# Kernel tuning notes

Measured on AMD Instinct MI355X. Metric: run time of the kernel, lower is better.

The kernel has to match this reference:

```python
import jax, jax.numpy as jnp
import numpy as np

B, T, G, H = 4, 2048, 1024, 16
HD = G // H  # head dim = 64


def setup_inputs() -> dict:
    key = jax.random.key(0)
    ks = jax.random.split(key, 5)
    s = 1.0 / np.sqrt(G).astype(np.float32)
    return {
        "x": jax.random.normal(ks[0], (B, T, G), jnp.float32),
        "wq": jax.random.normal(ks[1], (G, G), jnp.float32) * s,
        "bq": jnp.zeros((G,), jnp.float32),
        "wk": jax.random.normal(ks[2], (G, G), jnp.float32) * s,
        "bk": jnp.zeros((G,), jnp.float32),
        "wv": jax.random.normal(ks[3], (G, G), jnp.float32) * s,
        "bv": jnp.zeros((G,), jnp.float32),
        "wp": jax.random.normal(ks[4], (G, G), jnp.float32) * s,
        "bp": jnp.zeros((G,), jnp.float32),
    }


def reference(x, wq, bq, wk, bk, wv, bv, wp, bp):
    b, t, g = x.shape
    # QKV projections -> [B, H, T, HD]
    def split_heads(y):
        return y.reshape(b, t, H, HD).transpose(0, 2, 1, 3)
    q = split_heads(x @ wq + bq)
    k = split_heads(x @ wk + bk)
    v = split_heads(x @ wv + bv)
    scale = 1.0 / np.sqrt(HD).astype(np.float32)
    att = jnp.einsum("bhqd,bhkd->bhqk", q, k) * scale  # [B,H,T,T]
    causal = jnp.tril(jnp.ones((t, t), bool))
    att = jnp.where(causal[None, None], att, -jnp.inf)
    att = jax.nn.softmax(att, axis=-1)
    y = jnp.einsum("bhqk,bhkd->bhqd", att, v)  # [B,H,T,HD]
    y = y.transpose(0, 2, 1, 3).reshape(b, t, g)
    return y @ wp + bp
```

## Files before the change

kernel.cpp:

```cpp
#include <hip/hip_runtime.h>
#include <hip/hip_bf16.h>
#include <stdint.h>

typedef unsigned short u16;
typedef __attribute__((ext_vector_type(4))) float f32x4;
typedef __attribute__((ext_vector_type(8))) __bf16 bf16x8;
typedef __attribute__((ext_vector_type(4))) __bf16 bf16x4;
typedef __attribute__((ext_vector_type(4))) unsigned int u32x4;

#define DEV __device__ __forceinline__

DEV u16 f2bf(float f){
  unsigned u = __builtin_bit_cast(unsigned, f);
  u += 0x7fffu + ((u >> 16) & 1u);
  return (u16)(u >> 16);
}

DEV float fexp2(float x){ float r; asm("v_exp_f32 %0, %1" : "=v"(r) : "v"(x)); return r; }

#define GL2LDS(g, l) __builtin_amdgcn_global_load_lds( \
    (const __attribute__((address_space(1))) unsigned int*)(g), \
    (__attribute__((address_space(3))) unsigned int*)(l), 16, 0, 0)

constexpr int Tt = 2048, Gg = 1024, HD = 64;
constexpr float LOG2E = 1.44269504088896340736f;

__global__ __launch_bounds__(256) void k_cvt_x(const float* __restrict__ x, u16* __restrict__ xb){
  long i = (long)blockIdx.x * 256 + threadIdx.x;
  const float4* p = (const float4*)x + 2 * i;
  float4 a = p[0], c = p[1];
  u32x4 v;
  v[0] = (unsigned)f2bf(a.x) | ((unsigned)f2bf(a.y) << 16);
  v[1] = (unsigned)f2bf(a.z) | ((unsigned)f2bf(a.w) << 16);
  v[2] = (unsigned)f2bf(c.x) | ((unsigned)f2bf(c.y) << 16);
  v[3] = (unsigned)f2bf(c.z) | ((unsigned)f2bf(c.w) << 16);
  *(u32x4*)(xb + 8 * i) = v;
}

__global__ void k_transW(const float* __restrict__ wq, const float* __restrict__ wk,
                         const float* __restrict__ wv, const float* __restrict__ wp,
                         u16* __restrict__ wqkvT, u16* __restrict__ wpT){
  __shared__ float tile[32][33];
  int z = blockIdx.z;
  const float* w = (z == 0) ? wq : (z == 1) ? wk : (z == 2) ? wv : wp;
  u16* o = (z < 3) ? (wqkvT + (size_t)z * Gg * Gg) : wpT;
  int n0 = blockIdx.x * 32, k0 = blockIdx.y * 32;
  for (int r = threadIdx.y; r < 32; r += 8)
    tile[r][threadIdx.x] = w[(size_t)(k0 + r) * Gg + n0 + threadIdx.x];
  __syncthreads();
  for (int r = threadIdx.y; r < 32; r += 8)
    o[(size_t)(n0 + r) * Gg + k0 + threadIdx.x] = f2bf(tile[threadIdx.x][r]);
}

template<int EPI>
__global__ __launch_bounds__(256) void k_gemm(
    const u16* __restrict__ A, const u16* __restrict__ Bt, int M, int N, int K,
    const float* __restrict__ b0, const float* __restrict__ b1, const float* __restrict__ b2,
    u16* __restrict__ q_out, u16* __restrict__ k_out, u16* __restrict__ v_out,
    float* __restrict__ out, const float* __restrict__ bp){
  __shared__ u16 lA[2][128 * 32];
  __shared__ u16 lB[2][128 * 32];
  const int tid = threadIdx.x;
  const int lane = tid & 63, w = tid >> 6;
  const int lr = lane & 15, lg = lane >> 4;
  const int wr = w >> 1, wc = w & 1;
  int bid = blockIdx.x;
  int cpx = gridDim.x >> 3;
  int sbid = (bid & 7) * cpx + (bid >> 3);
  const int nbn = N >> 7;
  const int mb = sbid / nbn, nb = sbid % nbn;
  const int m0 = mb * 128, n0 = nb * 128;

  f32x4 acc[4][4];
#pragma unroll
  for (int i = 0; i < 4; i++)
#pragma unroll
    for (int j = 0; j < 4; j++) acc[i][j] = (f32x4)0.f;

  const int lrow = lane >> 2;
  const int lch  = lane & 3;
  const int gswz = (lrow >> 2) & 3;
  const size_t aRow0 = (size_t)(m0 + w * 32 + lrow) * K + (lch ^ gswz) * 8;
  const size_t bRow0 = (size_t)(n0 + w * 32 + lrow) * K + (lch ^ gswz) * 8;

#pragma unroll
  for (int j = 0; j < 2; j++) {
    GL2LDS(A  + aRow0 + (size_t)j * 16 * K, &lA[0][(w * 32 + j * 16) * 32]);
    GL2LDS(Bt + bRow0 + (size_t)j * 16 * K, &lB[0][(w * 32 + j * 16) * 32]);
  }
  __syncthreads();

  int cur = 0;
  for (int k0 = 0; k0 < K; k0 += 32) {
    if (k0 + 32 < K) {
#pragma unroll
      for (int j = 0; j < 2; j++) {
        GL2LDS(A  + aRow0 + (size_t)j * 16 * K + k0 + 32, &lA[cur ^ 1][(w * 32 + j * 16) * 32]);
        GL2LDS(Bt + bRow0 + (size_t)j * 16 * K + k0 + 32, &lB[cur ^ 1][(w * 32 + j * 16) * 32]);
      }
    }
    bf16x8 af[4], bfr[4];
#pragma unroll
    for (int mi = 0; mi < 4; mi++) {
      int row = wr * 64 + mi * 16 + lr;
      int ch = lg ^ ((row >> 2) & 3);
      af[mi] = *(const bf16x8*)&lA[cur][row * 32 + ch * 8];
    }
#pragma unroll
    for (int nj = 0; nj < 4; nj++) {
      int row = wc * 64 + nj * 16 + lr;
      int ch = lg ^ ((row >> 2) & 3);
      bfr[nj] = *(const bf16x8*)&lB[cur][row * 32 + ch * 8];
    }
#pragma unroll
    for (int mi = 0; mi < 4; mi++)
#pragma unroll
      for (int nj = 0; nj < 4; nj++)
        acc[mi][nj] = __builtin_amdgcn_mfma_f32_16x16x32_bf16(af[mi], bfr[nj], acc[mi][nj], 0, 0, 0);

    __syncthreads();
    cur ^= 1;
  }

  if constexpr (EPI == 0) {
#pragma unroll
    for (int nj = 0; nj < 4; nj++) {
      int col = n0 + wc * 64 + nj * 16 + lr;
      int tsel = col >> 10;
      int nn = col & 1023;
      const float* bptr = (tsel == 0) ? b0 : (tsel == 1) ? b1 : b2;
      float bias = bptr[nn];
      int h = nn >> 6, d = nn & 63;
      if (tsel == 2) {
#pragma unroll
        for (int mi = 0; mi < 4; mi++) {
          int rowb = m0 + wr * 64 + mi * 16 + lg * 4;
          int bb = rowb >> 11, t = rowb & 2047;
          int bh = bb * 16 + h;
          ushort4 pk;
          pk.x = f2bf(acc[mi][nj][0] + bias);
          pk.y = f2bf(acc[mi][nj][1] + bias);
          pk.z = f2bf(acc[mi][nj][2] + bias);
          pk.w = f2bf(acc[mi][nj][3] + bias);
          *(ushort4*)&v_out[((size_t)bh * 64 + d) * 2048 + t] = pk;
        }
      } else {
        u16* dst = (tsel == 0) ? q_out : k_out;
        const float sc = (tsel == 0) ? 0.125f * LOG2E : 1.0f;
#pragma unroll
        for (int mi = 0; mi < 4; mi++) {
          int rowb = m0 + wr * 64 + mi * 16 + lg * 4;
#pragma unroll
          for (int r = 0; r < 4; r++) {
            int row = rowb + r;
            int bb = row >> 11, t = row & 2047;
            float v = (acc[mi][nj][r] + bias) * sc;
            dst[((size_t)(bb * 16 + h) * 2048 + t) * 64 + d] = f2bf(v);
          }
        }
      }
    }
  } else {
#pragma unroll
    for (int nj = 0; nj < 4; nj++) {
      int col = n0 + wc * 64 + nj * 16 + lr;
      float bias = bp[col];
#pragma unroll
      for (int mi = 0; mi < 4; mi++) {
#pragma unroll
        for (int r = 0; r < 4; r++) {
          int row = m0 + wr * 64 + mi * 16 + lg * 4 + r;
          out[(size_t)row * 1024 + col] = acc[mi][nj][r] + bias;
        }
      }
    }
  }
}

__global__ __launch_bounds__(512, 4) void k_attn(const u16* __restrict__ Qb, const u16* __restrict__ Kb,
                                                 const u16* __restrict__ Vtb, u16* __restrict__ Ob){
  __shared__ u16 lK[2][64 * 64];
  __shared__ u16 lV[2][64 * 64];
  __shared__ u16 plds[8][1024];
  const int tid = threadIdx.x, lane = tid & 63, w = tid >> 6;
  const int lr = lane & 15, lg = lane >> 4;
  const int slot = blockIdx.x & 255;
  const int rr = blockIdx.x >> 8;
  const int bh = slot & 63;
  const int g  = slot >> 6;
  const int qb = (rr == 0) ? 7 - g : g;
  const int q0w = qb * 256 + w * 32;
  const int b = bh >> 4, h = bh & 15;
  const size_t base  = (size_t)bh * Tt * HD;
  const size_t vbase = (size_t)bh * HD * Tt;
  char* pw = (char*)&plds[w][0];

  const int sl3 = lane >> 3, sc = lane & 7;
  const int r0 = w * 8;
  const int srow = r0 + sl3;
  const int schk = (sc ^ (srow & 7)) * 8;

  bf16x8 qf[2][2];
#pragma unroll
  for (int qg = 0; qg < 2; qg++)
#pragma unroll
    for (int dh = 0; dh < 2; dh++)
      qf[qg][dh] = *(const bf16x8*)(Qb + base + (size_t)(q0w + qg * 16 + lr) * 64 + dh * 32 + lg * 8);

  f32x4 Oacc[2][4];
#pragma unroll
  for (int qg = 0; qg < 2; qg++)
#pragma unroll
    for (int nf = 0; nf < 4; nf++) Oacc[qg][nf] = (f32x4)0.f;
  float mrun[2] = {-__builtin_inff(), -__builtin_inff()};
  float lsum[2] = {0.f, 0.f};

  const int ntile = 4 * qb + 4;

  GL2LDS(Kb + base + (size_t)srow * 64 + schk, &lK[0][r0 * 64]);
  GL2LDS(Vtb + vbase + (size_t)srow * Tt + schk, &lV[0][r0 * 64]);
  __syncthreads();

  int cur = 0;
  for (int kt = 0; kt < ntile; kt++) {
    const int kv0 = kt << 6;
    if (kt + 1 < ntile) {
      const int nkv0 = kv0 + 64;
      GL2LDS(Kb + base + (size_t)(nkv0 + srow) * 64 + schk, &lK[cur ^ 1][r0 * 64]);
      GL2LDS(Vtb + vbase + (size_t)srow * Tt + nkv0 + schk, &lV[cur ^ 1][r0 * 64]);
    }

    if (kv0 <= q0w + 31) {
      const bool full = (kv0 + 63 <= q0w);
      const u16* lKc = &lK[cur][0];
      const u16* lVc = &lV[cur][0];

      f32x4 accs[4][2];
#pragma unroll
      for (int kg = 0; kg < 4; kg++) {
        int row = kg * 16 + lr;
        bf16x8 kf0 = *(const bf16x8*)&lKc[row * 64 + (lg ^ (row & 7)) * 8];
        bf16x8 kf1 = *(const bf16x8*)&lKc[row * 64 + ((4 + lg) ^ (row & 7)) * 8];
#pragma unroll
        for (int qg = 0; qg < 2; qg++) {
          accs[kg][qg] = __builtin_amdgcn_mfma_f32_16x16x32_bf16(kf0, qf[qg][0], (f32x4)0.f, 0, 0, 0);
          accs[kg][qg] = __builtin_amdgcn_mfma_f32_16x16x32_bf16(kf1, qf[qg][1], accs[kg][qg], 0, 0, 0);
        }
      }

      float pvv[2][4][4];
#pragma unroll
      for (int qg = 0; qg < 2; qg++) {
        const int q = q0w + qg * 16 + lr;
        float tm = -__builtin_inff();
#pragma unroll
        for (int kg = 0; kg < 4; kg++)
#pragma unroll
          for (int r = 0; r < 4; r++) {
            float s = accs[kg][qg][r];
            if (!full) { int kv = kv0 + kg * 16 + lg * 4 + r; if (kv > q) s = -__builtin_inff(); }
            pvv[qg][kg][r] = s;
            tm = fmaxf(tm, s);
          }
        if (!__all(tm <= mrun[qg] + 8.f)) {
          float tmr = fmaxf(tm, __shfl_xor(tm, 16));
          tmr = fmaxf(tmr, __shfl_xor(tmr, 32));
          float mnew = fmaxf(mrun[qg], tmr);
          float alpha = fexp2(mrun[qg] - mnew);
          mrun[qg] = mnew;
          lsum[qg] *= alpha;
#pragma unroll
          for (int r = 0; r < 4; r++) {
            float aO = __shfl(alpha, lg * 4 + r);
#pragma unroll
            for (int nf = 0; nf < 4; nf++) Oacc[qg][nf][r] *= aO;
          }
        }
        const float m = mrun[qg];
        float ps = 0.f;
#pragma unroll
        for (int kg = 0; kg < 4; kg++)
#pragma unroll
          for (int r = 0; r < 4; r++) {
            float p = fexp2(pvv[qg][kg][r] - m);
            pvv[qg][kg][r] = p;
            ps += p;
          }
        lsum[qg] += ps;
      }

      bf16x8 vfr[2][4];
      const int rs = lr & 7;
#pragma unroll
      for (int qg = 0; qg < 2; qg++) {
#pragma unroll
        for (int kg = 0; kg < 4; kg++) {
          int chunk = kg * 2 + (lg >> 1);
          int byte = lr * 128 + ((chunk ^ rs) << 4) + (lg & 1) * 8;
          bf16x4 t;
          t[0] = (__bf16)pvv[qg][kg][0]; t[1] = (__bf16)pvv[qg][kg][1];
          t[2] = (__bf16)pvv[qg][kg][2]; t[3] = (__bf16)pvv[qg][kg][3];
          *(bf16x4*)(pw + byte) = t;
        }
#pragma unroll
        for (int ks = 0; ks < 2; ks++) {
          bf16x8 pf = *(const bf16x8*)(pw + lr * 128 + (((ks * 4 + lg) ^ rs) << 4));
#pragma unroll
          for (int nf = 0; nf < 4; nf++) {
            if (qg == 0) {
              int vrow = nf * 16 + lr;
              vfr[ks][nf] = *(const bf16x8*)&lVc[vrow * 64 + ((ks * 4 + lg) ^ (vrow & 7)) * 8];
            }
            Oacc[qg][nf] = __builtin_amdgcn_mfma_f32_16x16x32_bf16(pf, vfr[ks][nf], Oacc[qg][nf], 0, 0, 0);
          }
        }
      }
    }

    __syncthreads();
    cur ^= 1;
  }

#pragma unroll
  for (int qg = 0; qg < 2; qg++) {
    float ls = lsum[qg];
    ls += __shfl_xor(ls, 16);
    ls += __shfl_xor(ls, 32);
    float li = 1.f / ls;
#pragma unroll
    for (int r = 0; r < 4; r++) {
      float liO = __shfl(li, lg * 4 + r);
      int q = q0w + qg * 16 + lg * 4 + r;
      size_t rowoff = ((size_t)b * Tt + q) * Gg + h * 64;
#pragma unroll
      for (int nf = 0; nf < 4; nf++)
        Ob[rowoff + nf * 16 + lr] = f2bf(Oacc[qg][nf][r] * liO);
    }
  }
}

extern "C" void kernel_launch(void* const* d_in, const int* in_sizes, int n_in,
                              void* d_out, int out_size, void* d_ws, size_t ws_size,
                              hipStream_t stream){
  const float* x  = (const float*)d_in[0];
  const float* wq = (const float*)d_in[1];
  const float* bq = (const float*)d_in[2];
  const float* wk = (const float*)d_in[3];
  const float* bk = (const float*)d_in[4];
  const float* wv = (const float*)d_in[5];
  const float* bv = (const float*)d_in[6];
  const float* wp = (const float*)d_in[7];
  const float* bp = (const float*)d_in[8];
  float* out = (float*)d_out;
  char* ws = (char*)d_ws;

  u16* xb    = (u16*)(ws);
  u16* wqkvT = (u16*)(ws + (16l << 20));
  u16* wpT   = (u16*)(ws + (22l << 20));
  u16* Qb    = (u16*)(ws + (24l << 20));
  u16* Kb    = (u16*)(ws + (40l << 20));
  u16* Vtb   = (u16*)(ws + (56l << 20));
  u16* Ao    = (u16*)(ws + (72l << 20));

  k_cvt_x<<<dim3(4096), dim3(256), 0, stream>>>(x, xb);
  k_transW<<<dim3(32, 32, 4), dim3(32, 8), 0, stream>>>(wq, wk, wv, wp, wqkvT, wpT);
  k_gemm<0><<<dim3(64 * 24), dim3(256), 0, stream>>>(xb, wqkvT, 8192, 3072, 1024,
                                                     bq, bk, bv, Qb, Kb, Vtb, nullptr, nullptr);
  k_attn<<<dim3(512), dim3(512), 0, stream>>>(Qb, Kb, Vtb, Ao);
  k_gemm<1><<<dim3(64 * 8), dim3(256), 0, stream>>>(Ao, wpT, 8192, 1024, 1024,
                                                    nullptr, nullptr, nullptr, nullptr, nullptr, nullptr,
                                                    out, bp);
}
```

Baseline: 183.0 us.

## Split attention work across 16 waves with 16 query rows each

The attention kernel now launches 1024 threads per block (16 waves), each wave owning 16 query rows instead of 32. K/V tile loads are split so waves 0-7 load K and waves 8-15 load V. The aim is more parallelism and latency hiding, plus fewer registers per wave. In exchange, each wave loses reuse of K and V fragments across two query groups, the per-wave P scratch in LDS doubles, and block-wide barriers now synchronise more waves.

Result: slower. 195.0 us (+6.6%).

```diff
diff --git a/kernel.cpp b/kernel.cpp
--- a/kernel.cpp
+++ b/kernel.cpp
@@ -177,11 +177,11 @@
   }
 }
 
-__global__ __launch_bounds__(512, 4) void k_attn(const u16* __restrict__ Qb, const u16* __restrict__ Kb,
-                                                 const u16* __restrict__ Vtb, u16* __restrict__ Ob){
+__global__ __launch_bounds__(1024, 8) void k_attn(const u16* __restrict__ Qb, const u16* __restrict__ Kb,
+                                                  const u16* __restrict__ Vtb, u16* __restrict__ Ob){
   __shared__ u16 lK[2][64 * 64];
   __shared__ u16 lV[2][64 * 64];
-  __shared__ u16 plds[8][1024];
+  __shared__ u16 plds[16][1024];
   const int tid = threadIdx.x, lane = tid & 63, w = tid >> 6;
   const int lr = lane & 15, lg = lane >> 4;
   const int slot = blockIdx.x & 255;
@@ -189,36 +189,33 @@
   const int bh = slot & 63;
   const int g  = slot >> 6;
   const int qb = (rr == 0) ? 7 - g : g;
-  const int q0w = qb * 256 + w * 32;
+  const int q0w = qb * 256 + w * 16;
   const int b = bh >> 4, h = bh & 15;
   const size_t base  = (size_t)bh * Tt * HD;
   const size_t vbase = (size_t)bh * HD * Tt;
   char* pw = (char*)&plds[w][0];
 
   const int sl3 = lane >> 3, sc = lane & 7;
-  const int r0 = w * 8;
+  const int r0 = (w & 7) * 8;
   const int srow = r0 + sl3;
   const int schk = (sc ^ (srow & 7)) * 8;
-
-  bf16x8 qf[2][2];
-#pragma unroll
-  for (int qg = 0; qg < 2; qg++)
-#pragma unroll
-    for (int dh = 0; dh < 2; dh++)
-      qf[qg][dh] = *(const bf16x8*)(Qb + base + (size_t)(q0w + qg * 16 + lr) * 64 + dh * 32 + lg * 8);
-
-  f32x4 Oacc[2][4];
-#pragma unroll
-  for (int qg = 0; qg < 2; qg++)
-#pragma unroll
-    for (int nf = 0; nf < 4; nf++) Oacc[qg][nf] = (f32x4)0.f;
-  float mrun[2] = {-__builtin_inff(), -__builtin_inff()};
-  float lsum[2] = {0.f, 0.f};
+  const bool isK = (w < 8);
+
+  bf16x8 qf[2];
+#pragma unroll
+  for (int dh = 0; dh < 2; dh++)
+    qf[dh] = *(const bf16x8*)(Qb + base + (size_t)(q0w + lr) * 64 + dh * 32 + lg * 8);
+
+  f32x4 Oacc[4];
+#pragma unroll
+  for (int nf = 0; nf < 4; nf++) Oacc[nf] = (f32x4)0.f;
+  float mrun = -__builtin_inff();
+  float lsum = 0.f;
 
   const int ntile = 4 * qb + 4;
 
-  GL2LDS(Kb + base + (size_t)srow * 64 + schk, &lK[0][r0 * 64]);
-  GL2LDS(Vtb + vbase + (size_t)srow * Tt + schk, &lV[0][r0 * 64]);
+  if (isK) GL2LDS(Kb + base + (size_t)srow * 64 + schk, &lK[0][r0 * 64]);
+  else     GL2LDS(Vtb + vbase + (size_t)srow * Tt + schk, &lV[0][r0 * 64]);
   __syncthreads();
 
   int cur = 0;
@@ -226,93 +223,83 @@
     const int kv0 = kt << 6;
     if (kt + 1 < ntile) {
       const int nkv0 = kv0 + 64;
-      GL2LDS(Kb + base + (size_t)(nkv0 + srow) * 64 + schk, &lK[cur ^ 1][r0 * 64]);
-      GL2LDS(Vtb + vbase + (size_t)srow * Tt + nkv0 + schk, &lV[cur ^ 1][r0 * 64]);
-    }
-
-    if (kv0 <= q0w + 31) {
+      if (isK) GL2LDS(Kb + base + (size_t)(nkv0 + srow) * 64 + schk, &lK[cur ^ 1][r0 * 64]);
+      else     GL2LDS(Vtb + vbase + (size_t)srow * Tt + nkv0 + schk, &lV[cur ^ 1][r0 * 64]);
+    }
+
+    if (kv0 <= q0w + 15) {
       const bool full = (kv0 + 63 <= q0w);
       const u16* lKc = &lK[cur][0];
       const u16* lVc = &lV[cur][0];
 
-      f32x4 accs[4][2];
+      f32x4 accs[4];
 #pragma unroll
       for (int kg = 0; kg < 4; kg++) {
         int row = kg * 16 + lr;
         bf16x8 kf0 = *(const bf16x8*)&lKc[row * 64 + (lg ^ (row & 7)) * 8];
         bf16x8 kf1 = *(const bf16x8*)&lKc[row * 64 + ((4 + lg) ^ (row & 7)) * 8];
-#pragma unroll
-        for (int qg = 0; qg < 2; qg++) {
-          accs[kg][qg] = __builtin_amdgcn_mfma_f32_16x16x32_bf16(kf0, qf[qg][0], (f32x4)0.f, 0, 0, 0);
-          accs[kg][qg] = __builtin_amdgcn_mfma_f32_16x16x32_bf16(kf1, qf[qg][1], accs[kg][qg], 0, 0, 0);
-        }
-      }
-
-      float pvv[2][4][4];
-#pragma unroll
-      for (int qg = 0; qg < 2; qg++) {
-        const int q = q0w + qg * 16 + lr;
+        accs[kg] = __builtin_amdgcn_mfma_f32_16x16x32_bf16(kf0, qf[0], (f32x4)0.f, 0, 0, 0);
+        accs[kg] = __builtin_amdgcn_mfma_f32_16x16x32_bf16(kf1, qf[1], accs[kg], 0, 0, 0);
+      }
+
+      float pvv[4][4];
+      {
+        const int q = q0w + lr;
         float tm = -__builtin_inff();
 #pragma unroll
         for (int kg = 0; kg < 4; kg++)
 #pragma unroll
           for (int r = 0; r < 4; r++) {
-            float s = accs[kg][qg][r];
+            float s = accs[kg][r];
             if (!full) { int kv = kv0 + kg * 16 + lg * 4 + r; if (kv > q) s = -__builtin_inff(); }
-            pvv[qg][kg][r] = s;
+            pvv[kg][r] = s;
             tm = fmaxf(tm, s);
           }
-        if (!__all(tm <= mrun[qg] + 8.f)) {
+        if (!__all(tm <= mrun + 8.f)) {
           float tmr = fmaxf(tm, __shfl_xor(tm, 16));
           tmr = fmaxf(tmr, __shfl_xor(tmr, 32));
-          float mnew = fmaxf(mrun[qg], tmr);
-          float alpha = fexp2(mrun[qg] - mnew);
-          mrun[qg] = mnew;
-          lsum[qg] *= alpha;
+          float mnew = fmaxf(mrun, tmr);
+          float alpha = fexp2(mrun - mnew);
+          mrun = mnew;
+          lsum *= alpha;
 #pragma unroll
           for (int r = 0; r < 4; r++) {
             float aO = __shfl(alpha, lg * 4 + r);
 #pragma unroll
-            for (int nf = 0; nf < 4; nf++) Oacc[qg][nf][r] *= aO;
+            for (int nf = 0; nf < 4; nf++) Oacc[nf][r] *= aO;
           }
         }
-        const float m = mrun[qg];
+        const float m = mrun;
         float ps = 0.f;
 #pragma unroll
         for (int kg = 0; kg < 4; kg++)
 #pragma unroll
           for (int r = 0; r < 4; r++) {
-            float p = fexp2(pvv[qg][kg][r] - m);
-            pvv[qg][kg][r] = p;
+            float p = fexp2(pvv[kg][r] - m);
+            pvv[kg][r] = p;
             ps += p;
           }
-        lsum[qg] += ps;
-      }
-
-      bf16x8 vfr[2][4];
+        lsum += ps;
+      }
+
       const int rs = lr & 7;
 #pragma unroll
-      for (int qg = 0; qg < 2; qg++) {
-#pragma unroll
-        for (int kg = 0; kg < 4; kg++) {
-          int chunk = kg * 2 + (lg >> 1);
-          int byte = lr * 128 + ((chunk ^ rs) << 4) + (lg & 1) * 8;
-          bf16x4 t;
-          t[0] = (__bf16)pvv[qg][kg][0]; t[1] = (__bf16)pvv[qg][kg][1];
-          t[2] = (__bf16)pvv[qg][kg][2]; t[3] = (__bf16)pvv[qg][kg][3];
-          *(bf16x4*)(pw + byte) = t;
-        }
-#pragma unroll
-        for (int ks = 0; ks < 2; ks++) {
-          bf16x8 pf = *(const bf16x8*)(pw + lr * 128 + (((ks * 4 + lg) ^ rs) << 4));
-#pragma unroll
-          for (int nf = 0; nf < 4; nf++) {
-            if (qg == 0) {
-              int vrow = nf * 16 + lr;
-              vfr[ks][nf] = *(const bf16x8*)&lVc[vrow * 64 + ((ks * 4 + lg) ^ (vrow & 7)) * 8];
-            }
-            Oacc[qg][nf] = __builtin_amdgcn_mfma_f32_16x16x32_bf16(pf, vfr[ks][nf], Oacc[qg][nf], 0, 0, 0);
-          }
+      for (int kg = 0; kg < 4; kg++) {
+        int chunk = kg * 2 + (lg >> 1);
+        int byte = lr * 128 + ((chunk ^ rs) << 4) + (lg & 1) * 8;
+        bf16x4 t;
+        t[0] = (__bf16)pvv[kg][0]; t[1] = (__bf16)pvv[kg][1];
+        t[2] = (__bf16)pvv[kg][2]; t[3] = (__bf16)pvv[kg][3];
+        *(bf16x4*)(pw + byte) = t;
+      }
+#pragma unroll
+      for (int ks = 0; ks < 2; ks++) {
+        bf16x8 pf = *(const bf16x8*)(pw + lr * 128 + (((ks * 4 + lg) ^ rs) << 4));
+#pragma unroll
+        for (int nf = 0; nf < 4; nf++) {
+          int vrow = nf * 16 + lr;
+          bf16x8 vf = *(const bf16x8*)&lVc[vrow * 64 + ((ks * 4 + lg) ^ (vrow & 7)) * 8];
+          Oacc[nf] = __builtin_amdgcn_mfma_f32_16x16x32_bf16(pf, vf, Oacc[nf], 0, 0, 0);
         }
       }
     }
@@ -321,20 +308,19 @@
     cur ^= 1;
   }
 
-#pragma unroll
-  for (int qg = 0; qg < 2; qg++) {
-    float ls = lsum[qg];
+  {
+    float ls = lsum;
     ls += __shfl_xor(ls, 16);
     ls += __shfl_xor(ls, 32);
     float li = 1.f / ls;
 #pragma unroll
     for (int r = 0; r < 4; r++) {
       float liO = __shfl(li, lg * 4 + r);
-      int q = q0w + qg * 16 + lg * 4 + r;
+      int q = q0w + lg * 4 + r;
       size_t rowoff = ((size_t)b * Tt + q) * Gg + h * 64;
 #pragma unroll
       for (int nf = 0; nf < 4; nf++)
-        Ob[rowoff + nf * 16 + lr] = f2bf(Oacc[qg][nf][r] * liO);
+        Ob[rowoff + nf * 16 + lr] = f2bf(Oacc[nf][r] * liO);
     }
   }
 }
@@ -366,7 +352,7 @@
   k_transW<<<dim3(32, 32, 4), dim3(32, 8), 0, stream>>>(wq, wk, wv, wp, wqkvT, wpT);
   k_gemm<0><<<dim3(64 * 24), dim3(256), 0, stream>>>(xb, wqkvT, 8192, 3072, 1024,
                                                      bq, bk, bv, Qb, Kb, Vtb, nullptr, nullptr);
-  k_attn<<<dim3(512), dim3(512), 0, stream>>>(Qb, Kb, Vtb, Ao);
+  k_attn<<<dim3(512), dim3(1024), 0, stream>>>(Qb, Kb, Vtb, Ao);
   k_gemm<1><<<dim3(64 * 8), dim3(256), 0, stream>>>(Ao, wpT, 8192, 1024, 1024,
                                                     nullptr, nullptr, nullptr, nullptr, nullptr, nullptr,
                                                     out, bp);
```
